# Kernel optimization log

Measured on AMD Instinct MI355X. Metric: run time of the kernel, lower is better.

The kernel has to match this reference:

```python
import jax, jax.numpy as jnp
import numpy as np
from jax import lax

K = 100  # topk kept per image


def _cxcywh_to_xyxy(b):
    cx, cy, w, h = b[..., 0], b[..., 1], b[..., 2], b[..., 3]
    return jnp.stack([cx - 0.5 * w, cy - 0.5 * h, cx + 0.5 * w, cy + 0.5 * h], axis=-1)


def setup_inputs() -> dict:
    key = jax.random.key(0)
    ks = jax.random.split(key, 7)
    B, Q, C, A = 32, 2000, 91, 18
    return {
        "pred_logits": jax.random.normal(ks[0], (B, Q, C), dtype=jnp.float32),
        "pred_boxes": jax.random.uniform(ks[1], (B, Q, 4), dtype=jnp.float32),
        "pred_adj": jax.random.normal(ks[2], (B, Q, Q), dtype=jnp.float32),
        "pred_logits_grasp": jax.random.normal(ks[3], (B, Q, C), dtype=jnp.float32),
        "pred_angles_grasp": jax.random.normal(ks[4], (B, Q, A), dtype=jnp.float32),
        "pred_boxes_grasp": jax.random.uniform(ks[5], (B, Q, 4), dtype=jnp.float32),
        "target_sizes": jax.random.uniform(ks[6], (B, 2), dtype=jnp.float32) * 800.0 + 200.0,
    }


def reference(pred_logits, pred_boxes, pred_adj, pred_logits_grasp,
              pred_angles_grasp, pred_boxes_grasp, target_sizes):
    B, Q, C = pred_logits.shape
    Cg = pred_logits_grasp.shape[2]

    # grasp angle decode: argmax over 18 bins -> degrees
    prob_ang = jax.nn.sigmoid(pred_angles_grasp)
    ang_idx = jnp.argmax(prob_ang, axis=2)[..., None]                 # [B,Q,1]
    angle = ((ang_idx - 8) * 10 - 5).astype(pred_boxes_grasp.dtype)
    bbox_grasp = jnp.concatenate([pred_boxes_grasp, angle], axis=2)   # [B,Q,5]

    prob = jax.nn.sigmoid(pred_logits)
    prob_g = jax.nn.sigmoid(pred_logits_grasp)

    topk_v, topk_i = lax.top_k(prob.reshape(B, -1), K)                # [B,K]
    keep = topk_v > 0.3                                               # [B,K]
    topk_vg, topk_ig = lax.top_k(prob_g.reshape(B, -1), K)

    topk_boxes = topk_i // C                                          # query indices
    labels = topk_i % C
    topk_boxes_g = topk_ig // Cg
    labels_g = topk_ig % Cg

    # adjacency extraction: adj[b] = sigmoid(pred_adj[b][idx][:, idx]), masked by keep
    adj = jax.vmap(lambda A, idx: A[idx][:, idx])(pred_adj, topk_boxes)  # [B,K,K]
    adj = jax.nn.sigmoid(adj)
    pair_mask = keep[:, :, None] & keep[:, None, :]
    adj = jnp.where(pair_mask, adj, 0.0)
    labels_kept = jnp.where(keep, labels, -1)

    boxes = _cxcywh_to_xyxy(pred_boxes)                               # [B,Q,4]
    boxes = jnp.take_along_axis(boxes, topk_boxes[:, :, None], axis=1)       # [B,K,4]
    boxes_g = jnp.take_along_axis(bbox_grasp, topk_boxes_g[:, :, None], axis=1)  # [B,K,5]

    img_h, img_w = target_sizes[:, 0], target_sizes[:, 1]
    scale = jnp.stack([img_w, img_h, img_w, img_h], axis=1)           # [B,4]
    boxes = boxes * scale[:, None, :]
    ones = jnp.ones_like(img_w)
    scale_g = jnp.stack([img_w, img_h, img_w, img_h, ones], axis=1)   # [B,5]
    boxes_g = boxes_g * scale_g[:, None, :]

    return topk_v, labels_kept, boxes, topk_vg, labels_g, boxes_g, adj, keep
```

## Files before the change

kernel.cpp:

```cpp
#include <hip/hip_runtime.h>
#include <math.h>

#define BB 32
#define Q 2000
#define NC 91
#define NA 18
#define K 100
#define N (Q*NC)
#define N4 (N/4)
#define NBINS 4096
#define G 8
#define BLK1 512
#define CHUNK4 ((N4 + G - 1) / G)
#define CAPM 4096
#define CAP2 1024

#define O_V     0
#define O_LAB   3200
#define O_BOX   6400
#define O_VG    19200
#define O_LABG  22400
#define O_BG    25600
#define O_ADJ   41600
#define O_KEEP  361600

__device__ __forceinline__ unsigned okey(float f) {
    unsigned u = __float_as_uint(f);
    return (u & 0x80000000u) ? ~u : (u | 0x80000000u);
}

__device__ __forceinline__ float sigm(float x) { return 1.f / (1.f + expf(-x)); }

__global__ __launch_bounds__(BLK1) void topk_part(const float* __restrict__ logits,
                                                  const float* __restrict__ logits_g,
                                                  unsigned* __restrict__ cnt2,
                                                  float* __restrict__ gv,
                                                  int* __restrict__ gi,
                                                  int cap) {
    const int g  = blockIdx.x;
    const int bw = blockIdx.y;
    const int b = bw >> 1, which = bw & 1;
    const float4* s4 = (const float4*)((which ? logits_g : logits) + (size_t)b * N);
    const int i0 = g * CHUNK4;
    const int i1 = (i0 + CHUNK4 < N4) ? (i0 + CHUNK4) : N4;

    __shared__ unsigned hist[NBINS];
    __shared__ unsigned tsum[BLK1];
    __shared__ int s_thr;
    __shared__ unsigned s_cnt;

    const int tid = threadIdx.x;
    for (int i = tid; i < NBINS; i += BLK1) hist[i] = 0u;
    if (tid == 0) s_cnt = 0u;
    __syncthreads();

    for (int i = i0 + tid; i < i1; i += BLK1) {
        float4 v = s4[i];
        atomicAdd(&hist[okey(v.x) >> 20], 1u);
        atomicAdd(&hist[okey(v.y) >> 20], 1u);
        atomicAdd(&hist[okey(v.z) >> 20], 1u);
        atomicAdd(&hist[okey(v.w) >> 20], 1u);
    }
    __syncthreads();

    unsigned h[8];
    unsigned s = 0;
    #pragma unroll
    for (int k = 0; k < 8; ++k) { h[k] = hist[tid * 8 + k]; s += h[k]; }
    tsum[tid] = s;
    __syncthreads();
    for (int off = 1; off < BLK1; off <<= 1) {
        unsigned add = (tid + off < BLK1) ? tsum[tid + off] : 0u;
        __syncthreads();
        tsum[tid] += add;
        __syncthreads();
    }
    unsigned sfx = (tid == BLK1 - 1) ? 0u : tsum[tid + 1];
    #pragma unroll
    for (int k = 7; k >= 0; --k) {
        unsigned nxt = sfx;
        sfx += h[k];
        if (sfx >= (unsigned)K && nxt < (unsigned)K) s_thr = tid * 8 + k;
    }
    __syncthreads();

    const unsigned thr = (unsigned)s_thr;
    const size_t base = (size_t)(bw * G + g) * (size_t)cap;
    for (int i = i0 + tid; i < i1; i += BLK1) {
        float4 v = s4[i];
        float xs[4] = {v.x, v.y, v.z, v.w};
        #pragma unroll
        for (int u = 0; u < 4; ++u) {
            if ((okey(xs[u]) >> 20) >= thr) {
                unsigned p = atomicAdd(&s_cnt, 1u);
                if ((int)p < cap) { gv[base + p] = xs[u]; gi[base + p] = i * 4 + u; }
            }
        }
    }
    __syncthreads();
    if (tid == 0) {
        unsigned c = s_cnt;
        cnt2[bw * G + g] = (c < (unsigned)cap) ? c : (unsigned)cap;
    }
}

__global__ __launch_bounds__(1024) void topk_merge(const unsigned* __restrict__ cnt2,
                                                   const float* __restrict__ gv,
                                                   const int* __restrict__ gi,
                                                   const float* __restrict__ boxes_in,
                                                   const float* __restrict__ boxes_g_in,
                                                   const float* __restrict__ angles_in,
                                                   const float* __restrict__ tsz,
                                                   float* __restrict__ out,
                                                   int* __restrict__ ws_keep,
                                                   int* __restrict__ ws_q,
                                                   int cap) {
    const int bw = blockIdx.x;
    const int b = bw >> 1, which = bw & 1;

    __shared__ float cv[CAPM];
    __shared__ int   ci[CAPM];
    __shared__ unsigned hist[NBINS];
    __shared__ unsigned tsum[1024];
    __shared__ float sv[CAP2];
    __shared__ int   si[CAP2];
    __shared__ unsigned offs[G + 1];
    __shared__ int s_thr;
    __shared__ unsigned s_cnt;
    __shared__ float ovv[K];
    __shared__ int   ovi[K];

    const int tid = threadIdx.x;

    if (tid == 0) {
        unsigned o = 0;
        #pragma unroll
        for (int g2 = 0; g2 < G; ++g2) {
            offs[g2] = o;
            unsigned c = cnt2[bw * G + g2];
            o += (c < (unsigned)cap) ? c : (unsigned)cap;
        }
        offs[G] = o;
        s_cnt = 0u;
    }
    for (int i = tid; i < NBINS; i += 1024) hist[i] = 0u;
    __syncthreads();

    #pragma unroll
    for (int g2 = 0; g2 < G; ++g2) {
        const int o0 = (int)offs[g2];
        const int cg = (int)offs[g2 + 1] - o0;
        const size_t base = (size_t)(bw * G + g2) * (size_t)cap;
        for (int i = tid; i < cg; i += 1024) {
            const int dst = o0 + i;
            if (dst < CAPM) {
                float x = gv[base + i];
                cv[dst] = x;
                ci[dst] = gi[base + i];
                atomicAdd(&hist[okey(x) >> 20], 1u);
            }
        }
    }
    __syncthreads();

    unsigned h[4];
    unsigned s = 0;
    #pragma unroll
    for (int k = 0; k < 4; ++k) { h[k] = hist[tid * 4 + k]; s += h[k]; }
    tsum[tid] = s;
    __syncthreads();
    for (int off = 1; off < 1024; off <<= 1) {
        unsigned add = (tid + off < 1024) ? tsum[tid + off] : 0u;
        __syncthreads();
        tsum[tid] += add;
        __syncthreads();
    }
    unsigned sfx = (tid == 1023) ? 0u : tsum[tid + 1];
    #pragma unroll
    for (int k = 3; k >= 0; --k) {
        unsigned nxt = sfx;
        sfx += h[k];
        if (sfx >= (unsigned)K && nxt < (unsigned)K) s_thr = tid * 4 + k;
    }
    __syncthreads();

    const int cnt = (int)((offs[G] < (unsigned)CAPM) ? offs[G] : (unsigned)CAPM);
    const unsigned thr = (unsigned)s_thr;
    for (int i = tid; i < cnt; i += 1024) {
        if ((okey(cv[i]) >> 20) >= thr) {
            unsigned p = atomicAdd(&s_cnt, 1u);
            if (p < CAP2) { sv[p] = cv[i]; si[p] = ci[i]; }
        }
    }
    __syncthreads();

    const int c2 = (int)((s_cnt < (unsigned)CAP2) ? s_cnt : (unsigned)CAP2);
    for (int i = tid; i < c2; i += 1024) {
        const float vi = sv[i];
        const int ii = si[i];
        int r = 0;
        for (int j = 0; j < c2; ++j) {
            const float vj = sv[j];
            r += (vj > vi || (vj == vi && si[j] < ii)) ? 1 : 0;
        }
        if (r < K) { ovv[r] = vi; ovi[r] = ii; }
    }
    __syncthreads();

    if (tid < K) {
        const float Himg = tsz[b * 2 + 0];
        const float Wimg = tsz[b * 2 + 1];
        const float vlog = ovv[tid];
        const int idx = ovi[tid];
        const float sp = sigm(vlog);
        const int q = idx / NC;
        const int lab = idx - q * NC;
        if (which == 0) {
            const int keep = sp > 0.3f ? 1 : 0;
            out[O_V + b * K + tid] = sp;
            out[O_LAB + b * K + tid] = keep ? (float)lab : -1.f;
            const float* pb = boxes_in + ((size_t)b * Q + q) * 4;
            const float cx = pb[0], cy = pb[1], w = pb[2], hh = pb[3];
            float* ob = out + O_BOX + ((size_t)b * K + tid) * 4;
            ob[0] = (cx - 0.5f * w) * Wimg;
            ob[1] = (cy - 0.5f * hh) * Himg;
            ob[2] = (cx + 0.5f * w) * Wimg;
            ob[3] = (cy + 0.5f * hh) * Himg;
            out[O_KEEP + b * K + tid] = keep ? 1.f : 0.f;
            ws_keep[b * K + tid] = keep;
            ws_q[b * K + tid] = q;
        } else {
            out[O_VG + b * K + tid] = sp;
            out[O_LABG + b * K + tid] = (float)lab;
            const float* pg = boxes_g_in + ((size_t)b * Q + q) * 4;
            float* obg = out + O_BG + ((size_t)b * K + tid) * 5;
            obg[0] = pg[0] * Wimg;
            obg[1] = pg[1] * Himg;
            obg[2] = pg[2] * Wimg;
            obg[3] = pg[3] * Himg;
            const float* pa = angles_in + ((size_t)b * Q + q) * NA;
            int am = 0;
            float bv = pa[0];
            #pragma unroll
            for (int a = 1; a < NA; ++a) {
                const float x = pa[a];
                if (x > bv) { bv = x; am = a; }
            }
            obg[4] = (float)((am - 8) * 10 - 5);
        }
    }
}

__global__ void adj_kernel(const float* __restrict__ adj_in,
                           const int* __restrict__ ws_keep,
                           const int* __restrict__ ws_q,
                           float* __restrict__ out) {
    const int bi = blockIdx.x;
    const int b = bi / K;
    const int i = bi - b * K;
    const int j = threadIdx.x;
    if (j >= K) return;
    const int qi = ws_q[b * K + i];
    const int ki = ws_keep[b * K + i];
    const int qj = ws_q[b * K + j];
    const int kj = ws_keep[b * K + j];
    float val = 0.f;
    if (ki & kj) {
        const float a = adj_in[((size_t)b * Q + qi) * Q + qj];
        val = sigm(a);
    }
    out[O_ADJ + (size_t)bi * K + j] = val;
}

extern "C" void kernel_launch(void* const* d_in, const int* in_sizes, int n_in,
                              void* d_out, int out_size, void* d_ws, size_t ws_size,
                              hipStream_t stream) {
    const float* pred_logits   = (const float*)d_in[0];
    const float* pred_boxes    = (const float*)d_in[1];
    const float* pred_adj      = (const float*)d_in[2];
    const float* pred_logits_g = (const float*)d_in[3];
    const float* pred_angles_g = (const float*)d_in[4];
    const float* pred_boxes_g  = (const float*)d_in[5];
    const float* tsz           = (const float*)d_in[6];
    float* out = (float*)d_out;

    int* ws_keep = (int*)d_ws;
    int* ws_q    = ws_keep + 3200;
    unsigned* cnt2 = (unsigned*)(ws_q + 3200);
    size_t fixed = 3200 + 3200 + 512;
    size_t avail = ws_size / 4 > fixed ? ws_size / 4 - fixed : 0;
    int cap = (int)((avail / (64 * G * 2)) < 4096 ? (avail / (64 * G * 2)) : 4096);
    if (cap < 128) cap = 128;
    float* gv = (float*)(cnt2 + 512);
    int*   gi = (int*)(gv + (size_t)64 * G * cap);

    hipLaunchKernelGGL(topk_part, dim3(G, 64), dim3(BLK1), 0, stream,
                       pred_logits, pred_logits_g, cnt2, gv, gi, cap);
    hipLaunchKernelGGL(topk_merge, dim3(64), dim3(1024), 0, stream,
                       cnt2, gv, gi, pred_boxes, pred_boxes_g, pred_angles_g,
                       tsz, out, ws_keep, ws_q, cap);
    hipLaunchKernelGGL(adj_kernel, dim3(BB * K), dim3(128), 0, stream,
                       pred_adj, ws_keep, ws_q, out);
}
```

Baseline: 41.62 us.

## Cache per-vector max keys to skip reloads, double partition count, flatten adj grid

The partial top-k kernel now keeps the maximum histogram key of each float4 in registers during the histogram pass. In the compaction pass it reloads only the vectors that can hold a candidate, instead of re-reading the whole chunk. The grid doubles to 16 partitions per image with a fixed 512-slot candidate segment, which raises parallelism, and the merge buffer grows to match. The adjacency kernel is flattened to full 512-thread blocks with no idle lanes. The cost is more register pressure from the per-thread key array and a fixed per-segment cap that could drop candidates.

```diff
diff --git a/kernel.cpp b/kernel.cpp
--- a/kernel.cpp
+++ b/kernel.cpp
@@ -9,10 +9,12 @@
 #define N (Q*NC)
 #define N4 (N/4)
 #define NBINS 4096
-#define G 8
+#define G 16
 #define BLK1 512
 #define CHUNK4 ((N4 + G - 1) / G)
-#define CAPM 4096
+#define ITERS ((CHUNK4 + BLK1 - 1) / BLK1)
+#define CAPSEG 512
+#define CAPM 8192
 #define CAP2 1024
 
 #define O_V     0
@@ -35,8 +37,7 @@
                                                   const float* __restrict__ logits_g,
                                                   unsigned* __restrict__ cnt2,
                                                   float* __restrict__ gv,
-                                                  int* __restrict__ gi,
-                                                  int cap) {
+                                                  int* __restrict__ gi) {
     const int g  = blockIdx.x;
     const int bw = blockIdx.y;
     const int b = bw >> 1, which = bw & 1;
@@ -54,12 +55,26 @@
     if (tid == 0) s_cnt = 0u;
     __syncthreads();
 
-    for (int i = i0 + tid; i < i1; i += BLK1) {
-        float4 v = s4[i];
-        atomicAdd(&hist[okey(v.x) >> 20], 1u);
-        atomicAdd(&hist[okey(v.y) >> 20], 1u);
-        atomicAdd(&hist[okey(v.z) >> 20], 1u);
-        atomicAdd(&hist[okey(v.w) >> 20], 1u);
+    unsigned mk[ITERS];
+    #pragma unroll
+    for (int t = 0; t < ITERS; ++t) {
+        const int i = i0 + tid + t * BLK1;
+        unsigned m = 0u;
+        if (i < i1) {
+            float4 v = s4[i];
+            const unsigned k0 = okey(v.x) >> 20;
+            const unsigned k1 = okey(v.y) >> 20;
+            const unsigned k2 = okey(v.z) >> 20;
+            const unsigned k3 = okey(v.w) >> 20;
+            atomicAdd(&hist[k0], 1u);
+            atomicAdd(&hist[k1], 1u);
+            atomicAdd(&hist[k2], 1u);
+            atomicAdd(&hist[k3], 1u);
+            const unsigned m01 = k0 > k1 ? k0 : k1;
+            const unsigned m23 = k2 > k3 ? k2 : k3;
+            m = m01 > m23 ? m01 : m23;
+        }
+        mk[t] = m;
     }
     __syncthreads();
 
@@ -85,22 +100,26 @@
     __syncthreads();
 
     const unsigned thr = (unsigned)s_thr;
-    const size_t base = (size_t)(bw * G + g) * (size_t)cap;
-    for (int i = i0 + tid; i < i1; i += BLK1) {
-        float4 v = s4[i];
-        float xs[4] = {v.x, v.y, v.z, v.w};
-        #pragma unroll
-        for (int u = 0; u < 4; ++u) {
-            if ((okey(xs[u]) >> 20) >= thr) {
-                unsigned p = atomicAdd(&s_cnt, 1u);
-                if ((int)p < cap) { gv[base + p] = xs[u]; gi[base + p] = i * 4 + u; }
+    const size_t base = (size_t)(bw * G + g) * CAPSEG;
+    #pragma unroll
+    for (int t = 0; t < ITERS; ++t) {
+        if (mk[t] >= thr) {
+            const int i = i0 + tid + t * BLK1;
+            float4 v = s4[i];
+            float xs[4] = {v.x, v.y, v.z, v.w};
+            #pragma unroll
+            for (int u = 0; u < 4; ++u) {
+                if ((okey(xs[u]) >> 20) >= thr) {
+                    unsigned p = atomicAdd(&s_cnt, 1u);
+                    if (p < (unsigned)CAPSEG) { gv[base + p] = xs[u]; gi[base + p] = i * 4 + u; }
+                }
             }
         }
     }
     __syncthreads();
     if (tid == 0) {
         unsigned c = s_cnt;
-        cnt2[bw * G + g] = (c < (unsigned)cap) ? c : (unsigned)cap;
+        cnt2[bw * G + g] = (c < (unsigned)CAPSEG) ? c : (unsigned)CAPSEG;
     }
 }
 
@@ -113,8 +132,7 @@
                                                    const float* __restrict__ tsz,
                                                    float* __restrict__ out,
                                                    int* __restrict__ ws_keep,
-                                                   int* __restrict__ ws_q,
-                                                   int cap) {
+                                                   int* __restrict__ ws_q) {
     const int bw = blockIdx.x;
     const int b = bw >> 1, which = bw & 1;
 
@@ -137,8 +155,7 @@
         #pragma unroll
         for (int g2 = 0; g2 < G; ++g2) {
             offs[g2] = o;
-            unsigned c = cnt2[bw * G + g2];
-            o += (c < (unsigned)cap) ? c : (unsigned)cap;
+            o += cnt2[bw * G + g2];
         }
         offs[G] = o;
         s_cnt = 0u;
@@ -149,16 +166,13 @@
     #pragma unroll
     for (int g2 = 0; g2 < G; ++g2) {
         const int o0 = (int)offs[g2];
-        const int cg = (int)offs[g2 + 1] - o0;
-        const size_t base = (size_t)(bw * G + g2) * (size_t)cap;
-        for (int i = tid; i < cg; i += 1024) {
-            const int dst = o0 + i;
-            if (dst < CAPM) {
-                float x = gv[base + i];
-                cv[dst] = x;
-                ci[dst] = gi[base + i];
-                atomicAdd(&hist[okey(x) >> 20], 1u);
-            }
+        const int cg2 = (int)offs[g2 + 1] - o0;
+        const size_t base = (size_t)(bw * G + g2) * CAPSEG;
+        for (int i = tid; i < cg2; i += 1024) {
+            float x = gv[base + i];
+            cv[o0 + i] = x;
+            ci[o0 + i] = gi[base + i];
+            atomicAdd(&hist[okey(x) >> 20], 1u);
         }
     }
     __syncthreads();
@@ -184,12 +198,12 @@
     }
     __syncthreads();
 
-    const int cnt = (int)((offs[G] < (unsigned)CAPM) ? offs[G] : (unsigned)CAPM);
+    const int cnt = (int)offs[G];
     const unsigned thr = (unsigned)s_thr;
     for (int i = tid; i < cnt; i += 1024) {
         if ((okey(cv[i]) >> 20) >= thr) {
             unsigned p = atomicAdd(&s_cnt, 1u);
-            if (p < CAP2) { sv[p] = cv[i]; si[p] = ci[i]; }
+            if (p < (unsigned)CAP2) { sv[p] = cv[i]; si[p] = ci[i]; }
         }
     }
     __syncthreads();
@@ -251,25 +265,24 @@
     }
 }
 
-__global__ void adj_kernel(const float* __restrict__ adj_in,
-                           const int* __restrict__ ws_keep,
-                           const int* __restrict__ ws_q,
-                           float* __restrict__ out) {
-    const int bi = blockIdx.x;
-    const int b = bi / K;
-    const int i = bi - b * K;
-    const int j = threadIdx.x;
-    if (j >= K) return;
+__global__ __launch_bounds__(512) void adj_kernel(const float* __restrict__ adj_in,
+                                                  const int* __restrict__ ws_keep,
+                                                  const int* __restrict__ ws_q,
+                                                  float* __restrict__ out) {
+    const int idx = blockIdx.x * 512 + threadIdx.x;
+    const int b = idx / (K * K);
+    const int rem = idx - b * (K * K);
+    const int i = rem / K;
+    const int j = rem - i * K;
     const int qi = ws_q[b * K + i];
     const int ki = ws_keep[b * K + i];
     const int qj = ws_q[b * K + j];
     const int kj = ws_keep[b * K + j];
     float val = 0.f;
     if (ki & kj) {
-        const float a = adj_in[((size_t)b * Q + qi) * Q + qj];
-        val = sigm(a);
-    }
-    out[O_ADJ + (size_t)bi * K + j] = val;
+        val = sigm(adj_in[((size_t)b * Q + qi) * Q + qj]);
+    }
+    out[O_ADJ + idx] = val;
 }
 
 extern "C" void kernel_launch(void* const* d_in, const int* in_sizes, int n_in,
@@ -287,18 +300,14 @@
     int* ws_keep = (int*)d_ws;
     int* ws_q    = ws_keep + 3200;
     unsigned* cnt2 = (unsigned*)(ws_q + 3200);
-    size_t fixed = 3200 + 3200 + 512;
-    size_t avail = ws_size / 4 > fixed ? ws_size / 4 - fixed : 0;
-    int cap = (int)((avail / (64 * G * 2)) < 4096 ? (avail / (64 * G * 2)) : 4096);
-    if (cap < 128) cap = 128;
-    float* gv = (float*)(cnt2 + 512);
-    int*   gi = (int*)(gv + (size_t)64 * G * cap);
+    float* gv = (float*)(cnt2 + 64 * G);
+    int*   gi = (int*)(gv + (size_t)64 * G * CAPSEG);
 
     hipLaunchKernelGGL(topk_part, dim3(G, 64), dim3(BLK1), 0, stream,
-                       pred_logits, pred_logits_g, cnt2, gv, gi, cap);
+                       pred_logits, pred_logits_g, cnt2, gv, gi);
     hipLaunchKernelGGL(topk_merge, dim3(64), dim3(1024), 0, stream,
                        cnt2, gv, gi, pred_boxes, pred_boxes_g, pred_angles_g,
-                       tsz, out, ws_keep, ws_q, cap);
-    hipLaunchKernelGGL(adj_kernel, dim3(BB * K), dim3(128), 0, stream,
+                       tsz, out, ws_keep, ws_q);
+    hipLaunchKernelGGL(adj_kernel, dim3((BB * K * K) / 512), dim3(512), 0, stream,
                        pred_adj, ws_keep, ws_q, out);
 }
```

After: 42.99 us. 1.03x slower.
